# Kernel optimization log

Hardware: AMD Instinct MI355X
Metric: run time of the kernel (lower is better)

## Reference

```python
import jax, jax.numpy as jnp
import numpy as np

BN_EPS = 1e-5


def setup_inputs() -> dict:
    key = jax.random.key(0)
    k1, k2, k3 = jax.random.split(key, 3)
    B, C, H, W = 8, 1024, 48, 48
    Cb = 512
    x = jax.random.normal(k1, (B, C, H, W), dtype=jnp.float32)
    Wg = jax.random.normal(k2, (Cb, C), dtype=jnp.float32) * (1.0 / np.sqrt(C))
    Wz = jax.random.normal(k3, (C, Cb), dtype=jnp.float32) * (1.0 / np.sqrt(Cb))
    gamma = jnp.zeros((C,), dtype=jnp.float32)  # BN weight, const-init 0
    beta = jnp.zeros((C,), dtype=jnp.float32)   # BN bias,  const-init 0
    return {"x": x, "Wg": Wg, "Wz": Wz, "gamma": gamma, "beta": beta}


def reference(x, Wg, Wz, gamma, beta):
    B, C, H, W = x.shape
    HW = H * W
    xf = x.reshape(B, C, HW)                                  # [B,C,N]
    # attn[b,n,m] = <x[b,:,n], x[b,:,m]> / (H*W), softmax over m
    attn = jnp.einsum('bcn,bcm->bnm', xf, xf) / HW            # [B,N,N]
    attn = jax.nn.softmax(attn, axis=-1)
    # g: 1x1 conv C -> Cb (no bias)
    g = jnp.einsum('dc,bcn->bdn', Wg, xf)                     # [B,Cb,N]
    # y[b,d,n] = sum_m attn[b,n,m] * g[b,d,m]
    y = jnp.einsum('bnm,bdm->bdn', attn, g)                   # [B,Cb,N]
    # W_z: 1x1 conv Cb -> C (no bias)
    wy = jnp.einsum('cd,bdn->bcn', Wz, y)                     # [B,C,N]
    # BatchNorm2d in training mode: batch stats over (B, N), biased variance
    mean = jnp.mean(wy, axis=(0, 2), keepdims=True)
    var = jnp.mean(jnp.square(wy - mean), axis=(0, 2), keepdims=True)
    wy_bn = (wy - mean) * jax.lax.rsqrt(var + BN_EPS)
    wy_bn = wy_bn * gamma[None, :, None] + beta[None, :, None]
    z = wy_bn.reshape(B, C, H, W) + x
    return z
```

## Files before the change

### kernel.cpp

```cpp
#include <hip/hip_runtime.h>
#include <hip/hip_bf16.h>
#include <stdint.h>


typedef __bf16 bf16;
typedef __attribute__((ext_vector_type(8))) __bf16 bf16x8;
typedef __attribute__((ext_vector_type(4))) __bf16 bf16x4;
typedef __attribute__((ext_vector_type(4))) float f32x4;

template <bool F32OUT, bool BNRED, bool BXI, bool SMAXB>
__global__ __launch_bounds__(256)
void gemm_btz(const bf16* __restrict__ Ag, const bf16* __restrict__ Bg,
              void* __restrict__ Dg, int K, int N,
              long long sA, long long sB, long long sD, float alpha,
              float* __restrict__ ps, float* __restrict__ pq,
              const float* __restrict__ rsum, long long sR, int nInner, int nz)
{
    const int d  = blockIdx.x;
    const int zz = d % nz;
    const int t0 = d / nz;
    const int bI = t0 % nInner;
    const int bO = t0 / nInner;
    const int bx = BXI ? bI : bO;
    const int by = BXI ? bO : bI;

    __shared__ char lds[32768];
    char* ldsA = lds;
    char* ldsB = lds + 16384;

    const int lane = threadIdx.x & 63;
    const int wv   = threadIdx.x >> 6;
    const int wm   = wv >> 1;
    const int wn   = wv & 1;

    const bf16* Ab = Ag + (long long)zz * sA + (long long)by * 128 * K;
    const bf16* Bb = Bg + (long long)zz * sB + (long long)bx * 128 * K;

    float binv[4];
    if (SMAXB) {
        #pragma unroll
        for (int t = 0; t < 4; ++t) {
            int row = ((wv * 4 + t) * 64 + lane) >> 3;
            binv[t] = 1.0f / rsum[(long long)zz * sR + bx * 128 + row];
        }
    }

    f32x4 acc[4][4];
    #pragma unroll
    for (int i = 0; i < 4; ++i)
        #pragma unroll
        for (int j = 0; j < 4; ++j) {
            f32x4 z = {0.f, 0.f, 0.f, 0.f};
            acc[i][j] = z;
        }

    for (int k0 = 0; k0 < K; k0 += 64) {
        #pragma unroll
        for (int t = 0; t < 4; ++t) {
            int ch  = (wv * 4 + t) * 64 + lane;
            int row = ch >> 3;
            int cc  = (ch & 7) ^ (row & 7);
            bf16x8 va = *(const bf16x8*)(Ab + (long long)row * K + k0 + cc * 8);
            bf16x8 vb = *(const bf16x8*)(Bb + (long long)row * K + k0 + cc * 8);
            if (SMAXB) {
                #pragma unroll
                for (int q8 = 0; q8 < 8; ++q8)
                    vb[q8] = (bf16)((float)vb[q8] * binv[t]);
            }
            *(bf16x8*)(ldsA + ch * 16) = va;
            *(bf16x8*)(ldsB + ch * 16) = vb;
        }
        __syncthreads();

        #pragma unroll
        for (int kk = 0; kk < 64; kk += 32) {
            bf16x8 af[4], bfr[4];
            #pragma unroll
            for (int i = 0; i < 4; ++i) {
                int r = wm * 64 + i * 16 + (lane & 15);
                int c = ((kk >> 3) + (lane >> 4)) ^ (r & 7);
                af[i] = *(const bf16x8*)(ldsA + r * 128 + c * 16);
            }
            #pragma unroll
            for (int j = 0; j < 4; ++j) {
                int r = wn * 64 + j * 16 + (lane & 15);
                int c = ((kk >> 3) + (lane >> 4)) ^ (r & 7);
                bfr[j] = *(const bf16x8*)(ldsB + r * 128 + c * 16);
            }
            #pragma unroll
            for (int i = 0; i < 4; ++i)
                #pragma unroll
                for (int j = 0; j < 4; ++j)
                    acc[i][j] = __builtin_amdgcn_mfma_f32_16x16x32_bf16(af[i], bfr[j], acc[i][j], 0, 0, 0);
        }
        __syncthreads();
    }

    float* bs = (float*)lds;
    float* bq = (float*)(lds + 512);
    if (BNRED) {
        if (threadIdx.x < 128) { bs[threadIdx.x] = 0.f; bq[threadIdx.x] = 0.f; }
        __syncthreads();
    }

    const int m_base = by * 128 + wm * 64;
    const int n_base = bx * 128 + wn * 64;
    float s_it[4][4], q_it[4][4];
    #pragma unroll
    for (int i = 0; i < 4; ++i) {
        #pragma unroll
        for (int t = 0; t < 4; ++t) { s_it[i][t] = 0.f; q_it[i][t] = 0.f; }
    }
    #pragma unroll
    for (int i = 0; i < 4; ++i) {
        #pragma unroll
        for (int j = 0; j < 4; ++j) {
            int col = n_base + j * 16 + (lane & 15);
            #pragma unroll
            for (int t = 0; t < 4; ++t) {
                int rowg = m_base + i * 16 + (lane >> 4) * 4 + t;
                float v = acc[i][j][t] * alpha;
                if (F32OUT) ((float*)Dg)[(long long)zz * sD + (long long)rowg * N + col] = v;
                else        ((bf16*)Dg)[(long long)zz * sD + (long long)rowg * N + col] = (bf16)v;
                if (BNRED) { s_it[i][t] += v; q_it[i][t] += v * v; }
            }
        }
    }

    if (BNRED) {
        #pragma unroll
        for (int i = 0; i < 4; ++i) {
            #pragma unroll
            for (int t = 0; t < 4; ++t) {
                float s = s_it[i][t], q = q_it[i][t];
                #pragma unroll
                for (int m = 1; m < 16; m <<= 1) {
                    s += __shfl_xor(s, m);
                    q += __shfl_xor(q, m);
                }
                if ((lane & 15) == 0) {
                    int cl = wm * 64 + i * 16 + (lane >> 4) * 4 + t;
                    atomicAdd(&bs[cl], s);
                    atomicAdd(&bq[cl], q);
                }
            }
        }
        __syncthreads();
        if (threadIdx.x < 128) {
            int cg = by * 128 + threadIdx.x;
            atomicAdd(&ps[cg], bs[threadIdx.x]);
            atomicAdd(&pq[cg], bq[threadIdx.x]);
        }
    }
}

__global__ __launch_bounds__(256)
void gemm_sym(const bf16* __restrict__ Xg, bf16* __restrict__ Dg,
              int K, int N, long long sX, long long sD, float alpha,
              float* __restrict__ rsum)
{
    const int NZ = gridDim.z;
    const int d  = blockIdx.z * 171 + blockIdx.x;
    const int zz = d % NZ;
    int tlin     = d / NZ;
    int bi = 0;
    while (tlin >= 18 - bi) { tlin -= 18 - bi; ++bi; }
    const int bj = bi + tlin;
    const bool mir  = (bj > bi);
    const bool diag = (bj == bi);

    __shared__ __align__(16) char lds[35840];
    char* ldsA = lds;
    char* ldsB = diag ? lds : (lds + 16384);

    const int lane = threadIdx.x & 63;
    const int wv   = threadIdx.x >> 6;
    const int wm   = wv >> 1;
    const int wn   = wv & 1;

    const bf16* Ab = Xg + (long long)zz * sX + (long long)bi * 128 * K;
    const bf16* Bb = Xg + (long long)zz * sX + (long long)bj * 128 * K;

    f32x4 acc[4][4];
    #pragma unroll
    for (int i = 0; i < 4; ++i)
        #pragma unroll
        for (int j = 0; j < 4; ++j) {
            f32x4 z = {0.f, 0.f, 0.f, 0.f};
            acc[i][j] = z;
        }

    for (int k0 = 0; k0 < K; k0 += 64) {
        #pragma unroll
        for (int t = 0; t < 4; ++t) {
            int ch  = (wv * 4 + t) * 64 + lane;
            int row = ch >> 3;
            int cc  = (ch & 7) ^ (row & 7);
            bf16x8 va = *(const bf16x8*)(Ab + (long long)row * K + k0 + cc * 8);
            *(bf16x8*)(ldsA + ch * 16) = va;
            if (!diag) {
                bf16x8 vb = *(const bf16x8*)(Bb + (long long)row * K + k0 + cc * 8);
                *(bf16x8*)(ldsB + ch * 16) = vb;
            }
        }
        __syncthreads();

        #pragma unroll
        for (int kk = 0; kk < 64; kk += 32) {
            bf16x8 af[4], bfr[4];
            #pragma unroll
            for (int i = 0; i < 4; ++i) {
                int r = wm * 64 + i * 16 + (lane & 15);
                int c = ((kk >> 3) + (lane >> 4)) ^ (r & 7);
                af[i] = *(const bf16x8*)(ldsA + r * 128 + c * 16);
            }
            #pragma unroll
            for (int j = 0; j < 4; ++j) {
                int r = wn * 64 + j * 16 + (lane & 15);
                int c = ((kk >> 3) + (lane >> 4)) ^ (r & 7);
                bfr[j] = *(const bf16x8*)(ldsB + r * 128 + c * 16);
            }
            #pragma unroll
            for (int i = 0; i < 4; ++i)
                #pragma unroll
                for (int j = 0; j < 4; ++j)
                    acc[i][j] = __builtin_amdgcn_mfma_f32_16x16x32_bf16(af[i], bfr[j], acc[i][j], 0, 0, 0);
        }
        __syncthreads();
    }

    bf16* Db = Dg + (long long)zz * sD;
    float* rs = rsum + (long long)zz * N;
    bf16 (*tr)[140] = (bf16(*)[140])lds;

    float rowsum[4][4];
    float colsum[4];
    #pragma unroll
    for (int i = 0; i < 4; ++i)
        #pragma unroll
        for (int t = 0; t < 4; ++t) rowsum[i][t] = 0.f;
    #pragma unroll
    for (int j = 0; j < 4; ++j) colsum[j] = 0.f;

    #pragma unroll
    for (int i = 0; i < 4; ++i) {
        #pragma unroll
        for (int j = 0; j < 4; ++j) {
            int c_loc = wn * 64 + j * 16 + (lane & 15);
            int col   = bj * 128 + c_loc;
            bf16x4 tv;
            #pragma unroll
            for (int t = 0; t < 4; ++t) {
                int r_loc = wm * 64 + i * 16 + (lane >> 4) * 4 + t;
                float e = __expf(acc[i][j][t] * alpha);
                bf16 eb = (bf16)e;
                Db[(long long)(bi * 128 + r_loc) * N + col] = eb;
                tv[t] = eb;
                rowsum[i][t] += e;
                colsum[j]    += e;
            }
            if (mir) {
                int r_base = wm * 64 + i * 16 + (lane >> 4) * 4;
                *(bf16x4*)(&tr[c_loc][r_base]) = tv;
            }
        }
    }

    #pragma unroll
    for (int i = 0; i < 4; ++i) {
        #pragma unroll
        for (int t = 0; t < 4; ++t) {
            float s = rowsum[i][t];
            s += __shfl_xor(s, 1); s += __shfl_xor(s, 2);
            s += __shfl_xor(s, 4); s += __shfl_xor(s, 8);
            if ((lane & 15) == 0)
                atomicAdd(&rs[bi * 128 + wm * 64 + i * 16 + (lane >> 4) * 4 + t], s);
        }
    }
    if (mir) {
        #pragma unroll
        for (int j = 0; j < 4; ++j) {
            float s = colsum[j];
            s += __shfl_xor(s, 16); s += __shfl_xor(s, 32);
            if (lane < 16)
                atomicAdd(&rs[bj * 128 + wn * 64 + j * 16 + lane], s);
        }
        __syncthreads();
        const int cc = threadIdx.x >> 1, hf = threadIdx.x & 1;
        const bf16* src = &tr[cc][hf * 64];
        bf16* dst = Db + (long long)(bj * 128 + cc) * N + bi * 128 + hf * 64;
        #pragma unroll
        for (int j2 = 0; j2 < 8; ++j2)
            *(bf16x8*)(dst + j2 * 8) = *(const bf16x8*)(src + j2 * 8);
    }
}

__global__ __launch_bounds__(256)
void prep(const float* __restrict__ Wg, const float* __restrict__ Wz,
          bf16* __restrict__ Wgb, bf16* __restrict__ Wzb, float* __restrict__ zp)
{
    const int b = blockIdx.x;
    if (b < 1024) {
        const float* in = (b < 512) ? Wg : Wz;
        bf16* out       = (b < 512) ? Wgb : Wzb;
        int idx = (((b & 511) * 256) + threadIdx.x) * 4;
        float4 v = *(const float4*)(in + idx);
        out[idx + 0] = (bf16)v.x;
        out[idx + 1] = (bf16)v.y;
        out[idx + 2] = (bf16)v.z;
        out[idx + 3] = (bf16)v.w;
    } else {
        int i = ((b - 1024) * 256 + threadIdx.x) * 4;
        float4 z = {0.f, 0.f, 0.f, 0.f};
        *(float4*)(zp + i) = z;
    }
}

__global__ __launch_bounds__(256)
void zero_f32(float* __restrict__ p)
{
    p[blockIdx.x * 256 + threadIdx.x] = 0.f;
}

__global__ __launch_bounds__(256)
void transpose_f32_bf16(const float* __restrict__ x, bf16* __restrict__ xT)
{
    __shared__ bf16 tile[32][33];
    const float* xb = x + (long long)blockIdx.z * 1024 * 2304;
    bf16* xo = xT + (long long)blockIdx.z * 2304 * 1024;
    const int n0 = blockIdx.x * 32;
    const int c0 = blockIdx.y * 32;
    const int tx = threadIdx.x, ty = threadIdx.y;
    #pragma unroll
    for (int i = 0; i < 32; i += 8)
        tile[ty + i][tx] = (bf16)xb[(long long)(c0 + ty + i) * 2304 + n0 + tx];
    __syncthreads();
    #pragma unroll
    for (int i = 0; i < 32; i += 8)
        xo[(long long)(n0 + ty + i) * 1024 + c0 + tx] = tile[tx][ty + i];
}

__global__ __launch_bounds__(256)
void bn_apply_b(const bf16* __restrict__ wy, const float* __restrict__ x,
                const float* __restrict__ gamma, const float* __restrict__ beta,
                const float* __restrict__ ps, const float* __restrict__ pq,
                float* __restrict__ z)
{
    long long idx = ((long long)blockIdx.x * 256 + threadIdx.x) * 8;
    int c = (int)((idx / 2304) & 1023);
    float mu = ps[c] * (1.0f / 18432.0f);
    float is = rsqrtf(pq[c] * (1.0f / 18432.0f) - mu * mu + 1e-5f);
    float sc = gamma[c] * is;
    float sh = beta[c] - mu * sc;
    bf16x8 w  = *(const bf16x8*)(wy + idx);
    float4 x0 = *(const float4*)(x + idx);
    float4 x1 = *(const float4*)(x + idx + 4);
    float4 o0, o1;
    o0.x = (float)w[0] * sc + sh + x0.x;
    o0.y = (float)w[1] * sc + sh + x0.y;
    o0.z = (float)w[2] * sc + sh + x0.z;
    o0.w = (float)w[3] * sc + sh + x0.w;
    o1.x = (float)w[4] * sc + sh + x1.x;
    o1.y = (float)w[5] * sc + sh + x1.y;
    o1.z = (float)w[6] * sc + sh + x1.z;
    o1.w = (float)w[7] * sc + sh + x1.w;
    *(float4*)(z + idx)     = o0;
    *(float4*)(z + idx + 4) = o1;
}

extern "C" void kernel_launch(void* const* d_in, const int* in_sizes, int n_in,
                              void* d_out, int out_size, void* d_ws, size_t ws_size,
                              hipStream_t stream)
{
    const float* x     = (const float*)d_in[0];
    const float* Wg    = (const float*)d_in[1];
    const float* Wz    = (const float*)d_in[2];
    const float* gamma = (const float*)d_in[3];
    const float* beta  = (const float*)d_in[4];
    float* zo = (float*)d_out;

    const int B = 8, C = 1024, Cb = 512, N = 2304;

    const size_t fixedB = ((size_t)Cb * C * 2) * 2 + (size_t)C * 4 * 2 + (size_t)B * N * 4 + 4096;
    const size_t perB   = ((size_t)N * C + (size_t)Cb * N + (size_t)N * N + (size_t)N * Cb
                           + (size_t)C * N) * 2 + 1536;
    int BC = 8;
    while (BC > 1 && fixedB + perB * (size_t)BC > ws_size) BC >>= 1;

    char* p = (char*)d_ws;
    auto alloc = [&](size_t bytes) { char* r = p; p += (bytes + 255) & ~(size_t)255; return r; };
    bf16*  Wgb  = (bf16*)alloc((size_t)Cb * C * 2);
    bf16*  Wzb  = (bf16*)alloc((size_t)C * Cb * 2);
    float* psum = (float*)alloc((size_t)C * 4);
    float* pqsm = (float*)alloc((size_t)C * 4);
    float* rsum = (float*)alloc((size_t)B * N * 4);
    bf16*  xT   = (bf16*)alloc((size_t)BC * N * C * 2);
    bf16*  g    = (bf16*)alloc((size_t)BC * Cb * N * 2);
    bf16*  attn = (bf16*)alloc((size_t)BC * N * N * 2);
    bf16*  yT   = (bf16*)alloc((size_t)BC * N * Cb * 2);
    bf16*  wyb  = (bf16*)alloc((size_t)BC * C * N * 2);

    prep<<<dim3(1044), 256, 0, stream>>>(Wg, Wz, Wgb, Wzb, psum);

    for (int cs = 0; cs < B; cs += BC) {
        const float* xc = x + (long long)cs * C * N;

        if (BC < B && cs > 0)
            zero_f32<<<dim3((BC * N) / 256), 256, 0, stream>>>(rsum);

        transpose_f32_bf16<<<dim3(N / 32, C / 32, BC), dim3(32, 8), 0, stream>>>(xc, xT);

        gemm_btz<false, false, false, false><<<dim3(18 * 4 * BC), 256, 0, stream>>>(
            Wgb, xT, g, C, N, 0, (long long)N * C, (long long)Cb * N, 1.0f,
            nullptr, nullptr, nullptr, 0, 4, BC);

        gemm_sym<<<dim3(171, 1, BC), 256, 0, stream>>>(
            xT, attn, C, N, (long long)N * C, (long long)N * N, 1.0f / 2304.0f, rsum);

        gemm_btz<false, false, true, false><<<dim3(4 * 18 * BC), 256, 0, stream>>>(
            attn, g, yT, N, Cb, (long long)N * N, (long long)Cb * N, (long long)N * Cb, 1.0f,
            nullptr, nullptr, nullptr, 0, 4, BC);

        gemm_btz<false, true, false, true><<<dim3(18 * 8 * BC), 256, 0, stream>>>(
            Wzb, yT, wyb, Cb, N, 0, (long long)N * Cb, (long long)C * N, 1.0f,
            psum, pqsm, rsum, N, 8, BC);
    }

    if (BC == B) {
        bn_apply_b<<<dim3((B * C * N) / (256 * 8)), 256, 0, stream>>>(
            wyb, x, gamma, beta, psum, pqsm, zo);
    } else {
        for (int cs = 0; cs < B; cs += BC) {
            const float* xc = x + (long long)cs * C * N;
            float* zoc = zo + (long long)cs * C * N;
            zero_f32<<<dim3((BC * N) / 256), 256, 0, stream>>>(rsum);
            transpose_f32_bf16<<<dim3(N / 32, C / 32, BC), dim3(32, 8), 0, stream>>>(xc, xT);
            gemm_btz<false, false, false, false><<<dim3(18 * 4 * BC), 256, 0, stream>>>(
                Wgb, xT, g, C, N, 0, (long long)N * C, (long long)Cb * N, 1.0f,
                nullptr, nullptr, nullptr, 0, 4, BC);
            gemm_sym<<<dim3(171, 1, BC), 256, 0, stream>>>(
                xT, attn, C, N, (long long)N * C, (long long)N * N, 1.0f / 2304.0f, rsum);
            gemm_btz<false, false, true, false><<<dim3(4 * 18 * BC), 256, 0, stream>>>(
                attn, g, yT, N, Cb, (long long)N * N, (long long)Cb * N, (long long)N * Cb,
                1.0f, nullptr, nullptr, nullptr, 0, 4, BC);
            gemm_btz<false, false, false, true><<<dim3(18 * 8 * BC), 256, 0, stream>>>(
                Wzb, yT, wyb, Cb, N, 0, (long long)N * Cb, (long long)C * N, 1.0f,
                nullptr, nullptr, rsum, N, 8, BC);
            bn_apply_b<<<dim3((BC * C * N) / (256 * 8)), 256, 0, stream>>>(
                wyb, xc, gamma, beta, psum, pqsm, zoc);
        }
    }
}
```

Measured before the change: 380.5 us.

## Merge weight prep into transpose and run g-GEMM with attention GEMM in one launch

The weight bf16 conversion and stats zeroing are folded into extra blocks of the transpose kernel, removing a separate launch. The g projection GEMM and the symmetric attention GEMM are fused into one grid whose blocks dispatch to either body, so both independent GEMMs share the GPU and the launch gap between them disappears. In exchange every block of the fused kernel reserves the larger 35 KB LDS allocation, which may lower occupancy for the g-GEMM blocks, and the mixed grid may balance work unevenly.

```diff
diff --git a/kernel.cpp b/kernel.cpp
--- a/kernel.cpp
+++ b/kernel.cpp
@@ -9,14 +9,14 @@
 typedef __attribute__((ext_vector_type(4))) float f32x4;
 
 template <bool F32OUT, bool BNRED, bool BXI, bool SMAXB>
-__global__ __launch_bounds__(256)
-void gemm_btz(const bf16* __restrict__ Ag, const bf16* __restrict__ Bg,
+__device__ __forceinline__
+void btz_body(char* lds, int d,
+              const bf16* __restrict__ Ag, const bf16* __restrict__ Bg,
               void* __restrict__ Dg, int K, int N,
               long long sA, long long sB, long long sD, float alpha,
               float* __restrict__ ps, float* __restrict__ pq,
               const float* __restrict__ rsum, long long sR, int nInner, int nz)
 {
-    const int d  = blockIdx.x;
     const int zz = d % nz;
     const int t0 = d / nz;
     const int bI = t0 % nInner;
@@ -24,7 +24,6 @@
     const int bx = BXI ? bI : bO;
     const int by = BXI ? bO : bI;
 
-    __shared__ char lds[32768];
     char* ldsA = lds;
     char* ldsB = lds + 16384;
 
@@ -154,13 +153,12 @@
     }
 }
 
-__global__ __launch_bounds__(256)
-void gemm_sym(const bf16* __restrict__ Xg, bf16* __restrict__ Dg,
+__device__ __forceinline__
+void sym_body(char* lds, int d,
+              const bf16* __restrict__ Xg, bf16* __restrict__ Dg,
               int K, int N, long long sX, long long sD, float alpha,
-              float* __restrict__ rsum)
-{
-    const int NZ = gridDim.z;
-    const int d  = blockIdx.z * 171 + blockIdx.x;
+              float* __restrict__ rsum, int NZ)
+{
     const int zz = d % NZ;
     int tlin     = d / NZ;
     int bi = 0;
@@ -169,7 +167,6 @@
     const bool mir  = (bj > bi);
     const bool diag = (bj == bi);
 
-    __shared__ __align__(16) char lds[35840];
     char* ldsA = lds;
     char* ldsB = diag ? lds : (lds + 16384);
 
@@ -295,24 +292,85 @@
     }
 }
 
+template <bool F32OUT, bool BNRED, bool BXI, bool SMAXB>
 __global__ __launch_bounds__(256)
-void prep(const float* __restrict__ Wg, const float* __restrict__ Wz,
-          bf16* __restrict__ Wgb, bf16* __restrict__ Wzb, float* __restrict__ zp)
-{
-    const int b = blockIdx.x;
-    if (b < 1024) {
-        const float* in = (b < 512) ? Wg : Wz;
-        bf16* out       = (b < 512) ? Wgb : Wzb;
-        int idx = (((b & 511) * 256) + threadIdx.x) * 4;
-        float4 v = *(const float4*)(in + idx);
-        out[idx + 0] = (bf16)v.x;
-        out[idx + 1] = (bf16)v.y;
-        out[idx + 2] = (bf16)v.z;
-        out[idx + 3] = (bf16)v.w;
+void gemm_btz(const bf16* __restrict__ Ag, const bf16* __restrict__ Bg,
+              void* __restrict__ Dg, int K, int N,
+              long long sA, long long sB, long long sD, float alpha,
+              float* __restrict__ ps, float* __restrict__ pq,
+              const float* __restrict__ rsum, long long sR, int nInner, int nz)
+{
+    __shared__ char lds[32768];
+    btz_body<F32OUT, BNRED, BXI, SMAXB>(lds, blockIdx.x, Ag, Bg, Dg, K, N,
+                                        sA, sB, sD, alpha, ps, pq, rsum, sR, nInner, nz);
+}
+
+__global__ __launch_bounds__(256)
+void g_sym(const bf16* __restrict__ Wgb, const bf16* __restrict__ xT,
+           bf16* __restrict__ g, bf16* __restrict__ attn,
+           float* __restrict__ rsum, int nz)
+{
+    __shared__ __align__(16) char lds[35840];
+    const int NG = 72 * nz;
+    if ((int)blockIdx.x < NG) {
+        btz_body<false, false, false, false>(lds, blockIdx.x, Wgb, xT, g,
+            1024, 2304, 0, (long long)2304 * 1024, (long long)512 * 2304, 1.0f,
+            nullptr, nullptr, nullptr, 0, 4, nz);
     } else {
-        int i = ((b - 1024) * 256 + threadIdx.x) * 4;
-        float4 z = {0.f, 0.f, 0.f, 0.f};
-        *(float4*)(zp + i) = z;
+        sym_body(lds, (int)blockIdx.x - NG, xT, attn, 1024, 2304,
+                 (long long)2304 * 1024, (long long)2304 * 2304, 1.0f / 2304.0f,
+                 rsum, nz);
+    }
+}
+
+__global__ __launch_bounds__(256)
+void trans_prep(const float* __restrict__ x, bf16* __restrict__ xT,
+                const float* __restrict__ Wg, const float* __restrict__ Wz,
+                bf16* __restrict__ Wgb, bf16* __restrict__ Wzb,
+                float* __restrict__ zp, int doPrep)
+{
+    if (blockIdx.y < 32) {
+        __shared__ bf16 tile[32][33];
+        const float* xb = x + (long long)blockIdx.z * 1024 * 2304;
+        bf16* xo = xT + (long long)blockIdx.z * 2304 * 1024;
+        const int n0 = blockIdx.x * 32;
+        const int c0 = blockIdx.y * 32;
+        const int tx = threadIdx.x, ty = threadIdx.y;
+        #pragma unroll
+        for (int i = 0; i < 32; i += 8)
+            tile[ty + i][tx] = (bf16)xb[(long long)(c0 + ty + i) * 2304 + n0 + tx];
+        __syncthreads();
+        #pragma unroll
+        for (int i = 0; i < 32; i += 8)
+            xo[(long long)(n0 + ty + i) * 1024 + c0 + tx] = tile[tx][ty + i];
+        return;
+    }
+    if (!doPrep) return;
+    const int tid  = threadIdx.y * 32 + threadIdx.x;
+    const int strd = 72 * gridDim.z;
+    for (int pb = blockIdx.z * 72 + blockIdx.x; pb < 522; pb += strd) {
+        if (pb < 512) {
+            const float* in = (pb < 256) ? Wg : Wz;
+            bf16* out       = (pb < 256) ? Wgb : Wzb;
+            int base = (pb & 255) * 2048;
+            #pragma unroll
+            for (int h = 0; h < 2; ++h) {
+                int idx = base + h * 1024 + tid * 4;
+                float4 v = *(const float4*)(in + idx);
+                out[idx + 0] = (bf16)v.x;
+                out[idx + 1] = (bf16)v.y;
+                out[idx + 2] = (bf16)v.z;
+                out[idx + 3] = (bf16)v.w;
+            }
+        } else {
+            int base = (pb - 512) * 2048;
+            #pragma unroll
+            for (int h = 0; h < 2; ++h) {
+                int i = base + h * 1024 + tid * 4;
+                float4 z = {0.f, 0.f, 0.f, 0.f};
+                *(float4*)(zp + i) = z;
+            }
+        }
     }
 }
 
@@ -320,24 +378,6 @@
 void zero_f32(float* __restrict__ p)
 {
     p[blockIdx.x * 256 + threadIdx.x] = 0.f;
-}
-
-__global__ __launch_bounds__(256)
-void transpose_f32_bf16(const float* __restrict__ x, bf16* __restrict__ xT)
-{
-    __shared__ bf16 tile[32][33];
-    const float* xb = x + (long long)blockIdx.z * 1024 * 2304;
-    bf16* xo = xT + (long long)blockIdx.z * 2304 * 1024;
-    const int n0 = blockIdx.x * 32;
-    const int c0 = blockIdx.y * 32;
-    const int tx = threadIdx.x, ty = threadIdx.y;
-    #pragma unroll
-    for (int i = 0; i < 32; i += 8)
-        tile[ty + i][tx] = (bf16)xb[(long long)(c0 + ty + i) * 2304 + n0 + tx];
-    __syncthreads();
-    #pragma unroll
-    for (int i = 0; i < 32; i += 8)
-        xo[(long long)(n0 + ty + i) * 1024 + c0 + tx] = tile[tx][ty + i];
 }
 
 __global__ __launch_bounds__(256)
@@ -400,22 +440,16 @@
     bf16*  yT   = (bf16*)alloc((size_t)BC * N * Cb * 2);
     bf16*  wyb  = (bf16*)alloc((size_t)BC * C * N * 2);
 
-    prep<<<dim3(1044), 256, 0, stream>>>(Wg, Wz, Wgb, Wzb, psum);
-
     for (int cs = 0; cs < B; cs += BC) {
         const float* xc = x + (long long)cs * C * N;
 
         if (BC < B && cs > 0)
             zero_f32<<<dim3((BC * N) / 256), 256, 0, stream>>>(rsum);
 
-        transpose_f32_bf16<<<dim3(N / 32, C / 32, BC), dim3(32, 8), 0, stream>>>(xc, xT);
-
-        gemm_btz<false, false, false, false><<<dim3(18 * 4 * BC), 256, 0, stream>>>(
-            Wgb, xT, g, C, N, 0, (long long)N * C, (long long)Cb * N, 1.0f,
-            nullptr, nullptr, nullptr, 0, 4, BC);
-
-        gemm_sym<<<dim3(171, 1, BC), 256, 0, stream>>>(
-            xT, attn, C, N, (long long)N * C, (long long)N * N, 1.0f / 2304.0f, rsum);
+        trans_prep<<<dim3(N / 32, C / 32 + 1, BC), dim3(32, 8), 0, stream>>>(
+            xc, xT, Wg, Wz, Wgb, Wzb, psum, cs == 0 ? 1 : 0);
+
+        g_sym<<<dim3((72 + 171) * BC), 256, 0, stream>>>(Wgb, xT, g, attn, rsum, BC);
 
         gemm_btz<false, false, true, false><<<dim3(4 * 18 * BC), 256, 0, stream>>>(
             attn, g, yT, N, Cb, (long long)N * N, (long long)Cb * N, (long long)N * Cb, 1.0f,
@@ -434,12 +468,9 @@
             const float* xc = x + (long long)cs * C * N;
             float* zoc = zo + (long long)cs * C * N;
             zero_f32<<<dim3((BC * N) / 256), 256, 0, stream>>>(rsum);
-            transpose_f32_bf16<<<dim3(N / 32, C / 32, BC), dim3(32, 8), 0, stream>>>(xc, xT);
-            gemm_btz<false, false, false, false><<<dim3(18 * 4 * BC), 256, 0, stream>>>(
-                Wgb, xT, g, C, N, 0, (long long)N * C, (long long)Cb * N, 1.0f,
-                nullptr, nullptr, nullptr, 0, 4, BC);
-            gemm_sym<<<dim3(171, 1, BC), 256, 0, stream>>>(
-                xT, attn, C, N, (long long)N * C, (long long)N * N, 1.0f / 2304.0f, rsum);
+            trans_prep<<<dim3(N / 32, C / 32 + 1, BC), dim3(32, 8), 0, stream>>>(
+                xc, xT, Wg, Wz, Wgb, Wzb, psum, 0);
+            g_sym<<<dim3((72 + 171) * BC), 256, 0, stream>>>(Wgb, xT, g, attn, rsum, BC);
             gemm_btz<false, false, true, false><<<dim3(4 * 18 * BC), 256, 0, stream>>>(
                 attn, g, yT, N, Cb, (long long)N * N, (long long)Cb * N, (long long)N * Cb,
                 1.0f, nullptr, nullptr, nullptr, 0, 4, BC);
```

Measured after the change: 382.0 us. About the same (+0.4%).
